# Performance work log

Hardware: AMD Instinct MI355X
Metric: run time of the kernel (lower is better)

## Reference

```python
import jax, jax.numpy as jnp
import numpy as np

NUM_FREQ = 4
MAX_FREQ_LOG2 = 10.0
# standard NeRF frequency bands: 2^linspace(0, max_freq_log2, num_freq)
FREQ_BANDS = 2.0 ** np.linspace(0.0, MAX_FREQ_LOG2, NUM_FREQ).astype(np.float32)


def positional_encoding(x):
    # x: [N, 3] -> [N, 3*(1 + 2*num_freq)] = [N, 27]
    xf = x[..., None, :] * jnp.asarray(FREQ_BANDS, dtype=x.dtype)[:, None]  # [N, F, 3]
    enc = jnp.concatenate([jnp.sin(xf), jnp.cos(xf)], axis=-1)  # [N, F, 6]
    return jnp.concatenate([x, enc.reshape(x.shape[0], -1)], axis=-1)


def setup_inputs() -> dict:
    key = jax.random.key(0)
    k1, k2, k3 = jax.random.split(key, 3)
    N = 2097152
    x = jax.random.normal(k1, (N, 3), dtype=jnp.float32)
    in_dim, hidden = 27, 32
    # torch Linear default init scale ~ 1/sqrt(fan_in)
    W1 = jax.random.normal(k2, (in_dim, hidden), dtype=jnp.float32) / np.sqrt(in_dim)
    b1 = jnp.zeros((hidden,), dtype=jnp.float32)
    W2 = jax.random.normal(k3, (hidden, 1), dtype=jnp.float32) / np.sqrt(hidden)
    b2 = jnp.zeros((1,), dtype=jnp.float32)
    return {"x": x, "W1": W1, "b1": b1, "W2": W2, "b2": b2}


def reference(x, W1, b1, W2, b2):
    t = positional_encoding(x)                    # [N, 27]
    h = jax.nn.relu(t @ W1 + b1)                  # [N, 32]
    out = jax.nn.relu(h @ W2 + b2)                # [N, 1]
    return out
```

## Files before the change

### kernel.cpp

```cpp
#include <hip/hip_runtime.h>


#define NPTS  2097152
#define BLOCK 512
#define TILES 4
#define NBLK  (NPTS / (BLOCK * TILES))
#define TABN  4096

typedef __bf16 bf16x8 __attribute__((ext_vector_type(8)));
typedef __bf16 bf16x2 __attribute__((ext_vector_type(2)));
typedef float  f32x8  __attribute__((ext_vector_type(8)));
typedef float  f32x4  __attribute__((ext_vector_type(4)));
typedef float  f32x2  __attribute__((ext_vector_type(2)));
typedef unsigned int u32;
typedef u32 u32x4 __attribute__((ext_vector_type(4)));

__global__ __launch_bounds__(BLOCK, 4) void nerf_diet(
    const float* __restrict__ x,
    const float* __restrict__ W1,
    const float* __restrict__ b1,
    const float* __restrict__ W2,
    const float* __restrict__ b2,
    float* __restrict__ out)
{
    __shared__ u32 stab[TABN];
    __shared__ __align__(16) float ws[928];

    const int tid  = threadIdx.x;
    const int wave = tid >> 6;
    const int lane = tid & 63;
    const int g    = lane >> 4;
    const int c    = lane & 15;

    if (tid < 232) {
        float4 v;
        if (tid < 216)      v = ((const float4*)W1)[tid];
        else if (tid < 224) v = ((const float4*)b1)[tid - 216];
        else                v = ((const float4*)W2)[tid - 224];
        ((float4*)ws)[tid] = v;
    }

    #pragma unroll
    for (int i = 0; i < TABN / BLOCK; ++i) {
        const int idx = tid + i * BLOCK;
        const float a = (float)idx * (1.0f / TABN);
        f32x2 sc;
        sc[0] = __builtin_amdgcn_sinf(a);
        sc[1] = __builtin_amdgcn_cosf(a);
        stab[idx] = __builtin_bit_cast(u32, __builtin_convertvector(sc, bf16x2));
    }

    const float INV2PI = 0.15915494309189535f;
    float Fg = 1.0f;
    Fg = (g == 1) ? 10.079368f : Fg;
    Fg = (g == 2) ? 101.59367f : Fg;
    Fg = (g == 3) ? 1024.0f    : Fg;
    const float FgN4 = Fg * INV2PI * (float)TABN * 4.0f;

    const float bias2 = b2[0];
    const f32x4 Z = {0.f, 0.f, 0.f, 0.f};

    __syncthreads();

    bf16x8 afrag[2];
    #pragma unroll
    for (int mt = 0; mt < 2; ++mt) {
        const int j = mt * 16 + c;
        f32x8 af;
        #pragma unroll
        for (int m = 0; m < 3; ++m) {
            af[2 * m]     = ws[(3 + 6 * g + m) * 32 + j];
            af[2 * m + 1] = ws[(6 + 6 * g + m) * 32 + j];
        }
        af[6] = (g < 3) ? ws[g * 32 + j] : ws[864 + j];
        af[7] = 0.0f;
        afrag[mt] = __builtin_convertvector(af, bf16x8);
    }
    bf16x8 a2;
    {
        f32x8 a2f;
        #pragma unroll
        for (int i = 0; i < 4; ++i) {
            a2f[i]     = ws[896 + 4 * g + i];
            a2f[4 + i] = ws[896 + 16 + 4 * g + i];
        }
        a2 = __builtin_convertvector(a2f, bf16x8);
    }

    const char* stabB = (const char*)stab;
    const int tbase = blockIdx.x * ((BLOCK / 64) * TILES) + wave * TILES;
    const float* xb = x + (size_t)tbase * 192 + c * 3;
    float* ob = out + (size_t)tbase * 64 + lane;

    #pragma unroll
    for (int t = 0; t < TILES; ++t) {
        float p[4];
        #pragma unroll
        for (int nt = 0; nt < 4; ++nt) {
            const float x0 = xb[t * 192 + nt * 48 + 0];
            const float x1 = xb[t * 192 + nt * 48 + 1];
            const float x2 = xb[t * 192 + nt * 48 + 2];

            const u32 o0 = (u32)(int)(x0 * FgN4) & (4 * (TABN - 1));
            const u32 o1 = (u32)(int)(x1 * FgN4) & (4 * (TABN - 1));
            const u32 o2 = (u32)(int)(x2 * FgN4) & (4 * (TABN - 1));

            float extra = x0;
            extra = (g == 1) ? x1 : extra;
            extra = (g == 2) ? x2 : extra;
            extra = (g == 3) ? 1.0f : extra;

            u32x4 uu;
            uu[0] = *(const u32*)(stabB + o0);
            uu[1] = *(const u32*)(stabB + o1);
            uu[2] = *(const u32*)(stabB + o2);
            f32x2 ex = {extra, 0.0f};
            uu[3] = __builtin_bit_cast(u32, __builtin_convertvector(ex, bf16x2));
            const bf16x8 bf = __builtin_bit_cast(bf16x8, uu);

            const f32x4 acc0 =
                __builtin_amdgcn_mfma_f32_16x16x32_bf16(afrag[0], bf, Z, 0, 0, 0);
            const f32x4 acc1 =
                __builtin_amdgcn_mfma_f32_16x16x32_bf16(afrag[1], bf, Z, 0, 0, 0);

            f32x8 hf;
            #pragma unroll
            for (int rr = 0; rr < 2; ++rr) {
                f32x2 lo = {acc0[2 * rr], acc0[2 * rr + 1]};
                f32x2 hi = {acc1[2 * rr], acc1[2 * rr + 1]};
                f32x2 zz = {0.f, 0.f};
                lo = __builtin_elementwise_max(lo, zz);
                hi = __builtin_elementwise_max(hi, zz);
                hf[2 * rr] = lo[0]; hf[2 * rr + 1] = lo[1];
                hf[4 + 2 * rr] = hi[0]; hf[4 + 2 * rr + 1] = hi[1];
            }
            const bf16x8 h8 = __builtin_convertvector(hf, bf16x8);
            const f32x4 o =
                __builtin_amdgcn_mfma_f32_16x16x32_bf16(a2, h8, Z, 0, 0, 0);
            p[nt] = o[0];
        }

        float v = p[0];
        v = (g == 1) ? p[1] : v;
        v = (g == 2) ? p[2] : v;
        v = (g == 3) ? p[3] : v;
        ob[t * 64] = fmaxf(v + bias2, 0.0f);
    }
}

extern "C" void kernel_launch(void* const* d_in, const int* in_sizes, int n_in,
                              void* d_out, int out_size, void* d_ws, size_t ws_size,
                              hipStream_t stream) {
    const float* x  = (const float*)d_in[0];
    const float* W1 = (const float*)d_in[1];
    const float* b1 = (const float*)d_in[2];
    const float* W2 = (const float*)d_in[3];
    const float* b2 = (const float*)d_in[4];
    float* out = (float*)d_out;

    nerf_diet<<<NBLK, BLOCK, 0, stream>>>(x, W1, b1, W2, b2, out);
}
```

Measured before the change: 18.14 us.

## Switch first layer to 32x32x16 MFMA and do second layer with FMAs plus shuffle

Replaces the two 16x16x32 bf16 MFMAs per 16-point group with two chained 32x32x16 MFMAs per 32-point group. The K dimension is split across two half-waves, each handling two frequency bands. The second layer, which was a wasteful MFMA with only one useful output column, becomes per-lane packed FMAs against W2 followed by a cross-half-wave xor shuffle reduction. This is meant to cut MFMA count and the bf16 repacking of hidden activations, at the cost of a larger accumulator and more VALU work.

```diff
diff --git a/kernel.cpp b/kernel.cpp
--- a/kernel.cpp
+++ b/kernel.cpp
@@ -4,18 +4,18 @@
 #define NPTS  2097152
 #define BLOCK 512
 #define TILES 4
-#define NBLK  (NPTS / (BLOCK * TILES))
+#define NBLK  (NPTS / (64 * (BLOCK / 64) * TILES))
 #define TABN  4096
 
 typedef __bf16 bf16x8 __attribute__((ext_vector_type(8)));
 typedef __bf16 bf16x2 __attribute__((ext_vector_type(2)));
 typedef float  f32x8  __attribute__((ext_vector_type(8)));
-typedef float  f32x4  __attribute__((ext_vector_type(4)));
+typedef float  f32x16 __attribute__((ext_vector_type(16)));
 typedef float  f32x2  __attribute__((ext_vector_type(2)));
 typedef unsigned int u32;
 typedef u32 u32x4 __attribute__((ext_vector_type(4)));
 
-__global__ __launch_bounds__(BLOCK, 4) void nerf_diet(
+__global__ __launch_bounds__(BLOCK, 4) void nerf_32x32(
     const float* __restrict__ x,
     const float* __restrict__ W1,
     const float* __restrict__ b1,
@@ -29,8 +29,8 @@
     const int tid  = threadIdx.x;
     const int wave = tid >> 6;
     const int lane = tid & 63;
-    const int g    = lane >> 4;
-    const int c    = lane & 15;
+    const int h    = lane >> 5;
+    const int col  = lane & 31;
 
     if (tid < 232) {
         float4 v;
@@ -39,7 +39,6 @@
         else                v = ((const float4*)W2)[tid - 224];
         ((float4*)ws)[tid] = v;
     }
-
     #pragma unroll
     for (int i = 0; i < TABN / BLOCK; ++i) {
         const int idx = tid + i * BLOCK;
@@ -50,100 +49,90 @@
         stab[idx] = __builtin_bit_cast(u32, __builtin_convertvector(sc, bf16x2));
     }
 
-    const float INV2PI = 0.15915494309189535f;
-    float Fg = 1.0f;
-    Fg = (g == 1) ? 10.079368f : Fg;
-    Fg = (g == 2) ? 101.59367f : Fg;
-    Fg = (g == 3) ? 1024.0f    : Fg;
-    const float FgN4 = Fg * INV2PI * (float)TABN * 4.0f;
-
+    const float C4 = 0.15915494309189535f * (float)TABN * 4.0f;
+    const float FgA = (h ? 10.0793684f : 1.0f)        * C4;
+    const float FgB = (h ? 1024.0f     : 101.5936673f) * C4;
     const float bias2 = b2[0];
-    const f32x4 Z = {0.f, 0.f, 0.f, 0.f};
+    const f32x16 Z = {};
 
     __syncthreads();
 
-    bf16x8 afrag[2];
-    #pragma unroll
-    for (int mt = 0; mt < 2; ++mt) {
-        const int j = mt * 16 + c;
-        f32x8 af;
+    bf16x8 af1, af2;
+    {
+        f32x8 t1, t2;
         #pragma unroll
         for (int m = 0; m < 3; ++m) {
-            af[2 * m]     = ws[(3 + 6 * g + m) * 32 + j];
-            af[2 * m + 1] = ws[(6 + 6 * g + m) * 32 + j];
+            t1[2 * m]     = ws[(3  + 6 * h + m) * 32 + col];
+            t1[2 * m + 1] = ws[(6  + 6 * h + m) * 32 + col];
+            t2[2 * m]     = ws[(15 + 6 * h + m) * 32 + col];
+            t2[2 * m + 1] = ws[(18 + 6 * h + m) * 32 + col];
         }
-        af[6] = (g < 3) ? ws[g * 32 + j] : ws[864 + j];
-        af[7] = 0.0f;
-        afrag[mt] = __builtin_convertvector(af, bf16x8);
+        t1[6] = h ? ws[2 * 32 + col] : ws[0 * 32 + col];
+        t1[7] = h ? ws[864 + col]    : ws[1 * 32 + col];
+        t2[6] = 0.0f; t2[7] = 0.0f;
+        af1 = __builtin_convertvector(t1, bf16x8);
+        af2 = __builtin_convertvector(t2, bf16x8);
     }
-    bf16x8 a2;
-    {
-        f32x8 a2f;
-        #pragma unroll
-        for (int i = 0; i < 4; ++i) {
-            a2f[i]     = ws[896 + 4 * g + i];
-            a2f[4 + i] = ws[896 + 16 + 4 * g + i];
-        }
-        a2 = __builtin_convertvector(a2f, bf16x8);
+    f32x2 w2p[8];
+    #pragma unroll
+    for (int m = 0; m < 8; ++m) {
+        const int r0 = 896 + 8 * (m >> 1) + 4 * h + 2 * (m & 1);
+        w2p[m][0] = ws[r0];
+        w2p[m][1] = ws[r0 + 1];
     }
 
     const char* stabB = (const char*)stab;
     const int tbase = blockIdx.x * ((BLOCK / 64) * TILES) + wave * TILES;
-    const float* xb = x + (size_t)tbase * 192 + c * 3;
+    const float* xb = x + (size_t)tbase * 192 + col * 3;
     float* ob = out + (size_t)tbase * 64 + lane;
 
     #pragma unroll
     for (int t = 0; t < TILES; ++t) {
-        float p[4];
+        float S[2];
         #pragma unroll
-        for (int nt = 0; nt < 4; ++nt) {
-            const float x0 = xb[t * 192 + nt * 48 + 0];
-            const float x1 = xb[t * 192 + nt * 48 + 1];
-            const float x2 = xb[t * 192 + nt * 48 + 2];
+        for (int gr = 0; gr < 2; ++gr) {
+            const float x0 = xb[t * 192 + gr * 96 + 0];
+            const float x1 = xb[t * 192 + gr * 96 + 1];
+            const float x2 = xb[t * 192 + gr * 96 + 2];
 
-            const u32 o0 = (u32)(int)(x0 * FgN4) & (4 * (TABN - 1));
-            const u32 o1 = (u32)(int)(x1 * FgN4) & (4 * (TABN - 1));
-            const u32 o2 = (u32)(int)(x2 * FgN4) & (4 * (TABN - 1));
+            const u32 mA0 = (u32)(int)(x0 * FgA) & (4 * (TABN - 1));
+            const u32 mA1 = (u32)(int)(x1 * FgA) & (4 * (TABN - 1));
+            const u32 mA2 = (u32)(int)(x2 * FgA) & (4 * (TABN - 1));
+            const u32 mB0 = (u32)(int)(x0 * FgB) & (4 * (TABN - 1));
+            const u32 mB1 = (u32)(int)(x1 * FgB) & (4 * (TABN - 1));
+            const u32 mB2 = (u32)(int)(x2 * FgB) & (4 * (TABN - 1));
 
-            float extra = x0;
-            extra = (g == 1) ? x1 : extra;
-            extra = (g == 2) ? x2 : extra;
-            extra = (g == 3) ? 1.0f : extra;
+            u32x4 u1, u2;
+            u1[0] = *(const u32*)(stabB + mA0);
+            u1[1] = *(const u32*)(stabB + mA1);
+            u1[2] = *(const u32*)(stabB + mA2);
+            f32x2 ex;
+            ex[0] = h ? x2 : x0;
+            ex[1] = h ? 1.0f : x1;
+            u1[3] = __builtin_bit_cast(u32, __builtin_convertvector(ex, bf16x2));
+            u2[0] = *(const u32*)(stabB + mB0);
+            u2[1] = *(const u32*)(stabB + mB1);
+            u2[2] = *(const u32*)(stabB + mB2);
+            u2[3] = 0u;
+            const bf16x8 B1 = __builtin_bit_cast(bf16x8, u1);
+            const bf16x8 B2 = __builtin_bit_cast(bf16x8, u2);
 
-            u32x4 uu;
-            uu[0] = *(const u32*)(stabB + o0);
-            uu[1] = *(const u32*)(stabB + o1);
-            uu[2] = *(const u32*)(stabB + o2);
-            f32x2 ex = {extra, 0.0f};
-            uu[3] = __builtin_bit_cast(u32, __builtin_convertvector(ex, bf16x2));
-            const bf16x8 bf = __builtin_bit_cast(bf16x8, uu);
+            f32x16 acc = __builtin_amdgcn_mfma_f32_32x32x16_bf16(af1, B1, Z, 0, 0, 0);
+            acc = __builtin_amdgcn_mfma_f32_32x32x16_bf16(af2, B2, acc, 0, 0, 0);
 
-            const f32x4 acc0 =
-                __builtin_amdgcn_mfma_f32_16x16x32_bf16(afrag[0], bf, Z, 0, 0, 0);
-            const f32x4 acc1 =
-                __builtin_amdgcn_mfma_f32_16x16x32_bf16(afrag[1], bf, Z, 0, 0, 0);
-
-            f32x8 hf;
+            f32x2 ps = {0.0f, 0.0f};
             #pragma unroll
-            for (int rr = 0; rr < 2; ++rr) {
-                f32x2 lo = {acc0[2 * rr], acc0[2 * rr + 1]};
-                f32x2 hi = {acc1[2 * rr], acc1[2 * rr + 1]};
+            for (int m = 0; m < 8; ++m) {
+                f32x2 v = {acc[2 * m], acc[2 * m + 1]};
                 f32x2 zz = {0.f, 0.f};
-                lo = __builtin_elementwise_max(lo, zz);
-                hi = __builtin_elementwise_max(hi, zz);
-                hf[2 * rr] = lo[0]; hf[2 * rr + 1] = lo[1];
-                hf[4 + 2 * rr] = hi[0]; hf[4 + 2 * rr + 1] = hi[1];
+                v = __builtin_elementwise_max(v, zz);
+                ps = ps + v * w2p[m];
             }
-            const bf16x8 h8 = __builtin_convertvector(hf, bf16x8);
-            const f32x4 o =
-                __builtin_amdgcn_mfma_f32_16x16x32_bf16(a2, h8, Z, 0, 0, 0);
-            p[nt] = o[0];
+            float s = ps[0] + ps[1];
+            s += __shfl_xor(s, 32, 64);
+            S[gr] = s;
         }
-
-        float v = p[0];
-        v = (g == 1) ? p[1] : v;
-        v = (g == 2) ? p[2] : v;
-        v = (g == 3) ? p[3] : v;
+        const float v = h ? S[1] : S[0];
         ob[t * 64] = fmaxf(v + bias2, 0.0f);
     }
 }
@@ -158,5 +147,5 @@
     const float* b2 = (const float*)d_in[4];
     float* out = (float*)d_out;
 
-    nerf_diet<<<NBLK, BLOCK, 0, stream>>>(x, W1, b1, W2, b2, out);
+    nerf_32x32<<<NBLK, BLOCK, 0, stream>>>(x, W1, b1, W2, b2, out);
 }
```

Result: no change. 17.99 us (-0.9%).
